# Kernel optimization log

Measured on AMD Instinct MI355X. Metric: run time of the kernel, lower is better.

Reference implementation:

```python
import jax, jax.numpy as jnp
import numpy as np
from jax import lax

VOCAB, ENC_DIM, PRED_H, JOINT_H = 4096, 1024, 640, 640
T, MAX_SYM, BLANK, SOS = 128, 30, 0, -1
S = T * (MAX_SYM + 1)  # upper bound on greedy-decode loop iterations


def setup_inputs() -> dict:
    key = jax.random.key(0)
    ks = jax.random.split(key, 10)
    rn = lambda k, shape, s: jax.random.normal(k, shape, jnp.float32) * s
    return {
        "enc_out": rn(ks[0], (1, T, ENC_DIM), 1.0),
        "out_len": T,
        "emb": rn(ks[1], (VOCAB, PRED_H), 0.1),
        "Wih0": rn(ks[2], (4 * PRED_H, PRED_H), 0.04),
        "Whh0": rn(ks[3], (4 * PRED_H, PRED_H), 0.04),
        "b0": jnp.zeros((4 * PRED_H,), jnp.float32),
        "Wih1": rn(ks[4], (4 * PRED_H, PRED_H), 0.04),
        "Whh1": rn(ks[5], (4 * PRED_H, PRED_H), 0.04),
        "b1": jnp.zeros((4 * PRED_H,), jnp.float32),
        "Wj1": rn(ks[6], (JOINT_H, ENC_DIM + PRED_H), 0.03),
        "bj1": jnp.zeros((JOINT_H,), jnp.float32),
        "Wj2": rn(ks[7], (VOCAB, JOINT_H), 0.04),
        "bj2": jnp.zeros((VOCAB,), jnp.float32),
    }


def _lstm_cell(x, h, c, Wih, Whh, b):
    z = x @ Wih.T + h @ Whh.T + b  # [4H], torch gate order i,f,g,o
    i, f, g, o = jnp.split(z, 4)
    c2 = jax.nn.sigmoid(f) * c + jax.nn.sigmoid(i) * jnp.tanh(g)
    return jax.nn.sigmoid(o) * jnp.tanh(c2), c2


def _decode(enc_out, timesteps, emb, Wih0, Whh0, b0, Wih1, Whh1, b1, Wj1, bj1, Wj2, bj2):
    enc = enc_out[0]  # [T, ENC_DIM]

    def step(carry, _):
        t, sa, last, h0, c0, h1, c1, labels, cnt, done = carry
        # prediction net step (SOS = -1 -> zero embedding)
        g_in = jnp.where(last < 0, 0.0, emb[jnp.maximum(last, 0)])
        h0n, c0n = _lstm_cell(g_in, h0, c0, Wih0, Whh0, b0)
        h1n, c1n = _lstm_cell(h0n, h1, c1, Wih1, Whh1, b1)
        # joint net on current encoder frame
        f = enc[jnp.minimum(t, T - 1)]
        hid = jax.nn.relu(Wj1 @ jnp.concatenate([f, h1n]) + bj1)
        logits = Wj2 @ hid + bj2  # [VOCAB]
        k = jnp.argmax(logits).astype(jnp.int32)
        stop_sym = (k == BLANK) | (sa >= MAX_SYM)
        emit = (~stop_sym) & (~done)
        adv = stop_sym & (~done)
        # emit: append symbol, keep hidden'; blank/max: advance time, discard hidden'
        last2 = jnp.where(emit, k, last)
        h0 = jnp.where(emit, h0n, h0); c0 = jnp.where(emit, c0n, c0)
        h1 = jnp.where(emit, h1n, h1); c1 = jnp.where(emit, c1n, c1)
        labels = labels.at[cnt].set(jnp.where(emit, k, labels[cnt]))
        cnt2 = cnt + emit.astype(jnp.int32)
        sa2 = jnp.where(emit, sa + 1, jnp.where(adv, 0, sa))
        t2 = t + adv.astype(jnp.int32)
        done2 = done | (adv & (t2 >= timesteps))
        out_logits = jnp.where(done, 0.0, logits)
        return (t2, sa2, last2, h0, c0, h1, c1, labels, cnt2, done2), out_logits

    zeros = jnp.zeros((PRED_H,), jnp.float32)
    carry0 = (jnp.int32(0), jnp.int32(0), jnp.int32(SOS),
              zeros, zeros, zeros, zeros,
              jnp.full((S,), -1, jnp.int32), jnp.int32(0), jnp.bool_(False))
    carry, logits_seq = lax.scan(step, carry0, None, length=S)
    labels, cnt = carry[7], carry[8]
    return logits_seq, labels, cnt


def reference(enc_out, out_len, emb, Wih0, Whh0, b0, Wih1, Whh1, b1, Wj1, bj1, Wj2, bj2):
    return _decode(enc_out, out_len, emb, Wih0, Whh0, b0, Wih1, Whh1, b1, Wj1, bj1, Wj2, bj2)
```

## Files before the change

kernel.cpp:

```cpp
#include <hip/hip_runtime.h>
#include <cmath>

#define VOCAB   4096
#define ENC_DIM 1024
#define PRED_H  640
#define JOINT_H 640
#define TMAX    128
#define MAX_SYM 30
#define NSTEPS  (TMAX*(MAX_SYM+1))
#define NWG     160
#define NTHR    512
#define RLX __ATOMIC_RELAXED
#define AGT __HIP_MEMORY_SCOPE_AGENT

typedef unsigned long long u64;
typedef __attribute__((ext_vector_type(4))) float f32x4;
typedef __attribute__((ext_vector_type(4))) unsigned int u32x4;


__device__ __forceinline__ float wave_red(float v){
  v += __shfl_xor(v, 32, 64);
  v += __shfl_xor(v, 16, 64);
  v += __shfl_xor(v,  8, 64);
  v += __shfl_xor(v,  4, 64);
  v += __shfl_xor(v,  2, 64);
  v += __shfl_xor(v,  1, 64);
  return v;
}

__device__ __forceinline__ float sigf(float x){ return 1.0f/(1.0f+expf(-x)); }

__device__ __forceinline__ void sendline(u64* base, int w, f32x4 hv, unsigned tag){
  u32x4 a, b;
  a.x = __float_as_uint(hv.x); a.y = tag; a.z = __float_as_uint(hv.y); a.w = tag;
  b.x = __float_as_uint(hv.z); b.y = tag; b.z = __float_as_uint(hv.w); b.w = tag;
  u64* p = base + ((size_t)w<<3);
  asm volatile("global_store_dwordx4 %0, %2, off sc0 sc1\n\t"
               "global_store_dwordx4 %1, %3, off sc0 sc1"
               :: "v"(p), "v"(p+2), "v"(a), "v"(b) : "memory");
}

__device__ __forceinline__ void pollline(const u64* base, float* dstLDS,
                                         unsigned tag, int i){
  const u64* p = base + ((size_t)i<<3);
  u32x4 v0, v1;
  for(;;){
    asm volatile("global_load_dwordx4 %0, %2, off sc0 sc1\n\t"
                 "global_load_dwordx4 %1, %3, off sc0 sc1\n\t"
                 "s_waitcnt vmcnt(0)"
                 : "=&v"(v0), "=&v"(v1) : "v"(p), "v"(p+2) : "memory");
    if (v0.y == tag && v0.w == tag && v1.y == tag && v1.w == tag) break;
    __builtin_amdgcn_s_sleep(1);
  }
  __builtin_amdgcn_sched_barrier(0);
  float* d = dstLDS + (i<<2);
  d[0] = __uint_as_float(v0.x);
  d[1] = __uint_as_float(v0.z);
  d[2] = __uint_as_float(v1.x);
  d[3] = __uint_as_float(v1.z);
}

__device__ __forceinline__ u64 mkentry(float lg, int r, unsigned ep){
  unsigned u = __float_as_uint(lg);
  u = (u & 0x80000000u) ? ~u : (u | 0x80000000u);
  return ((u64)u<<24) | ((u64)(ep&0xFFFu)<<12) | (u64)(4095 - r);
}

__global__ void init_ws(unsigned* ws){
  for (int i = threadIdx.x; i < 10240; i += 256) ws[i] = 0u;
}

__global__ __launch_bounds__(NTHR, 1)
void rnnt_decode(const float* __restrict__ enc,
                 const int*   __restrict__ outlen_p,
                 const float* __restrict__ emb,
                 const float* __restrict__ Wih0, const float* __restrict__ Whh0, const float* __restrict__ b0,
                 const float* __restrict__ Wih1, const float* __restrict__ Whh1, const float* __restrict__ b1,
                 const float* __restrict__ Wj1,  const float* __restrict__ bj1,
                 const float* __restrict__ Wj2,  const float* __restrict__ bj2,
                 float* __restrict__ out,
                 char* __restrict__ ws)
{
  const int wg = blockIdx.x, tid = threadIdx.x;
  const int wave = tid >> 6, lane = tid & 63;
  const int timesteps = outlen_p[0];

  u64* dataA = (u64*)(ws);
  u64* dataB = (u64*)(ws + 10240);
  u64* dataH = (u64*)(ws + 20480);
  u64* parts = (u64*)(ws + 30720);

  __shared__ float xsh[ENC_DIM];
  __shared__ float h0buf[2][PRED_H];
  __shared__ float h1buf[2][PRED_H];
  __shared__ float hidsh[JOINT_H];
  __shared__ float zsh[4][4];
  __shared__ float zjsA[8], zjsB[8];
  __shared__ float c0c[4], c1c[4], c0p[4], c1p[4];
  __shared__ float bj1sh[4];
  __shared__ u64 psh[8];
  __shared__ u64 pmx[3];

  const int jb = wg*4;

  const int gA = wave & 3;
  const int jA = wave >> 2;
  const int rowA = gA*PRED_H + jb + jA;
  const int rowB = gA*PRED_H + jb + jA + 2;

  float w0xA[10], w0hA[10], w0xB[10], w0hB[10];
  float w1xA[10], w1hA[10], w1xB[10], w1hB[10];
  #pragma unroll
  for (int i = 0; i < 10; ++i){
    int c = lane + (i<<6);
    w0xA[i] = Wih0[(size_t)rowA*PRED_H + c];
    w0hA[i] = Whh0[(size_t)rowA*PRED_H + c];
    w1xA[i] = Wih1[(size_t)rowA*PRED_H + c];
    w1hA[i] = Whh1[(size_t)rowA*PRED_H + c];
    w0xB[i] = Wih0[(size_t)rowB*PRED_H + c];
    w0hB[i] = Whh0[(size_t)rowB*PRED_H + c];
    w1xB[i] = Wih1[(size_t)rowB*PRED_H + c];
    w1hB[i] = Whh1[(size_t)rowB*PRED_H + c];
  }
  const float bA0 = b0[rowA], bA1 = b1[rowA];
  const float bB0 = b0[rowB], bB1 = b1[rowB];

  const int grp = wave >> 2;
  const int vt  = ((wave & 3)<<6) | lane;
  const int rP0 = jb + grp;
  const int rP1 = jb + 2 + grp;
  float wjf0[4], wjh0[3], wjf1[4], wjh1[3];
  #pragma unroll
  for (int i = 0; i < 4; ++i){
    wjf0[i] = Wj1[(size_t)rP0*(ENC_DIM+PRED_H) + vt + (i<<8)];
    wjf1[i] = Wj1[(size_t)rP1*(ENC_DIM+PRED_H) + vt + (i<<8)];
  }
  #pragma unroll
  for (int i = 0; i < 3; ++i){
    int c = vt + (i<<8);
    wjh0[i] = (c < PRED_H) ? Wj1[(size_t)rP0*(ENC_DIM+PRED_H) + ENC_DIM + c] : 0.f;
    wjh1[i] = (c < PRED_H) ? Wj1[(size_t)rP1*(ENC_DIM+PRED_H) + ENC_DIM + c] : 0.f;
  }
  float ca0 = 0.f, ca1 = 0.f;

  const int nrows = (wg < 96) ? 26 : 25;
  const int r2b = wg*25 + (wg < 96 ? wg : 96);
  float wj2[4][10], bj2r[4];
  #pragma unroll
  for (int p = 0; p < 4; ++p){
    bool act = (p*8 + wave) < nrows;
    int r = act ? (r2b + p*8 + wave) : 0;
    #pragma unroll
    for (int i = 0; i < 10; ++i)
      wj2[p][i] = act ? Wj2[(size_t)r*JOINT_H + lane + (i<<6)] : 0.f;
    bj2r[p] = act ? bj2[r] : 0.f;
  }

  for (int i = tid; i < PRED_H; i += NTHR){ h0buf[0][i] = 0.f; h1buf[0][i] = 0.f;
                                            h0buf[1][i] = 0.f; h1buf[1][i] = 0.f; }
  if (tid < 4){ c0c[tid] = 0.f; c1c[tid] = 0.f; bj1sh[tid] = bj1[jb+tid]; }
  __syncthreads();

  int cur = 0, t = 0, sa = 0, last = -1, cnt = 0, tStaged = -1;
  bool done = false, reuse = false;
  float s0A = 0.f, s0B = 0.f, s1A = 0.f, s1B = 0.f;

  for (int s = 0; s < NSTEPS; ++s){
    if (done){
      if (wg < 8) out[(size_t)s*VOCAB + wg*NTHR + tid] = 0.f;
      continue;
    }
    const unsigned tag = (unsigned)(s + 1);

    if (!reuse){
      {
        float XA = 0.f, XB = 0.f;
        if (last >= 0){
          float xr[10];
          #pragma unroll
          for (int i = 0; i < 10; ++i)
            xr[i] = emb[(size_t)last*PRED_H + lane + (i<<6)];
          #pragma unroll
          for (int i = 0; i < 10; ++i){
            XA = fmaf(w0xA[i], xr[i], XA);
            XB = fmaf(w0xB[i], xr[i], XB);
          }
          XA = wave_red(XA);
          XB = wave_red(XB);
        }
        if (lane == 0){
          zsh[gA][jA]   = XA + s0A + bA0;
          zsh[gA][jA+2] = XB + s0B + bB0;
        }
      }
      __syncthreads();
      if (wave == 0){
        float hv = 0.f;
        if (lane < 4){
          float ig = sigf(zsh[0][lane]), fg = sigf(zsh[1][lane]);
          float gg = tanhf(zsh[2][lane]), og = sigf(zsh[3][lane]);
          float c2 = fg*c0c[lane] + ig*gg;
          c0p[lane] = c2;
          hv = og*tanhf(c2);
        }
        f32x4 v;
        v.x = __shfl(hv, 0, 64); v.y = __shfl(hv, 1, 64);
        v.z = __shfl(hv, 2, 64); v.w = __shfl(hv, 3, 64);
        if (lane == 0) sendline(dataA, wg, v, tag);
      }

      if (tid < 160) pollline(dataA, h0buf[cur^1], tag, tid);
      __syncthreads();
      {
        float XA = 0.f, XB = 0.f;
        #pragma unroll
        for (int i = 0; i < 10; ++i){
          float h0 = h0buf[cur^1][lane+(i<<6)];
          XA = fmaf(w1xA[i], h0, XA);
          XB = fmaf(w1xB[i], h0, XB);
        }
        XA = wave_red(XA);
        XB = wave_red(XB);
        if (lane == 0){
          zsh[gA][jA]   = XA + s1A + bA1;
          zsh[gA][jA+2] = XB + s1B + bB1;
        }
      }
      __syncthreads();
      if (wave == 0){
        float hv = 0.f;
        if (lane < 4){
          float ig = sigf(zsh[0][lane]), fg = sigf(zsh[1][lane]);
          float gg = tanhf(zsh[2][lane]), og = sigf(zsh[3][lane]);
          float c2 = fg*c1c[lane] + ig*gg;
          c1p[lane] = c2;
          hv = og*tanhf(c2);
        }
        f32x4 v;
        v.x = __shfl(hv, 0, 64); v.y = __shfl(hv, 1, 64);
        v.z = __shfl(hv, 2, 64); v.w = __shfl(hv, 3, 64);
        if (lane == 0) sendline(dataB, wg, v, tag);
      }
    }

    {
      int tcap = (t < TMAX-1) ? t : (TMAX-1);
      bool fNew = (tcap != tStaged);
      if (fNew)
        for (int i = tid; i < ENC_DIM; i += NTHR) xsh[i] = enc[(size_t)tcap*ENC_DIM + i];
      if (!reuse){
        if (tid < 160) pollline(dataB, h1buf[cur^1], tag, tid);
      }
      __syncthreads();
      if (fNew){
        float a = 0.f, b = 0.f;
        #pragma unroll
        for (int i = 0; i < 4; ++i){
          a = fmaf(wjf0[i], xsh[vt+(i<<8)], a);
          b = fmaf(wjf1[i], xsh[vt+(i<<8)], b);
        }
        ca0 = a; ca1 = b;
        tStaged = tcap;
      }
      {
        float acc = ca0;
        #pragma unroll
        for (int i = 0; i < 3; ++i){
          int c = vt + (i<<8);
          acc = fmaf(wjh0[i], h1buf[cur^1][(c < PRED_H) ? c : 0], acc);
        }
        acc = wave_red(acc);
        if (lane == 0) zjsA[wave] = acc;
        float acc2 = ca1;
        #pragma unroll
        for (int i = 0; i < 3; ++i){
          int c = vt + (i<<8);
          acc2 = fmaf(wjh1[i], h1buf[cur^1][(c < PRED_H) ? c : 0], acc2);
        }
        acc2 = wave_red(acc2);
        if (lane == 0) zjsB[wave] = acc2;
      }
      __syncthreads();
      if (wave == 0){
        float hv = 0.f;
        if (lane < 4){
          float v;
          if (lane == 0)      v = zjsA[0]+zjsA[1]+zjsA[2]+zjsA[3] + bj1sh[0];
          else if (lane == 1) v = zjsA[4]+zjsA[5]+zjsA[6]+zjsA[7] + bj1sh[1];
          else if (lane == 2) v = zjsB[0]+zjsB[1]+zjsB[2]+zjsB[3] + bj1sh[2];
          else                v = zjsB[4]+zjsB[5]+zjsB[6]+zjsB[7] + bj1sh[3];
          hv = v > 0.f ? v : 0.f;
        }
        f32x4 v;
        v.x = __shfl(hv, 0, 64); v.y = __shfl(hv, 1, 64);
        v.z = __shfl(hv, 2, 64); v.w = __shfl(hv, 3, 64);
        if (lane == 0) sendline(dataH, wg, v, tag);
      }
    }

    int k;
    {
      if (tid < 160) pollline(dataH, hidsh, tag, tid);
      __syncthreads();
      u64 best = 0;
      #pragma unroll
      for (int p = 0; p < 4; ++p){
        if (p*8 + wave < nrows){
          int r = r2b + p*8 + wave;
          float acc = 0.f;
          #pragma unroll
          for (int i = 0; i < 10; ++i) acc = fmaf(wj2[p][i], hidsh[lane+(i<<6)], acc);
          acc = wave_red(acc);
          if (lane == 0){
            float lg = acc + bj2r[p];
            out[(size_t)s*VOCAB + r] = lg;
            u64 e = mkentry(lg, r, tag);
            if (e > best) best = e;
          }
        }
      }
      if (lane == 0) psh[wave] = best;
      __syncthreads();
      if (tid == 0){
        u64 m = psh[0];
        #pragma unroll
        for (int w = 1; w < 8; ++w) if (psh[w] > m) m = psh[w];
        __hip_atomic_store(&parts[(size_t)wg<<3], m, RLX, AGT);
      }

      {
        float a0 = 0.f, b0v = 0.f, a1 = 0.f, b1v = 0.f;
        #pragma unroll
        for (int i = 0; i < 10; ++i){
          float h0p = h0buf[cur^1][lane+(i<<6)];
          float h1p = h1buf[cur^1][lane+(i<<6)];
          a0  = fmaf(w0hA[i], h0p, a0);
          b0v = fmaf(w0hB[i], h0p, b0v);
          a1  = fmaf(w1hA[i], h1p, a1);
          b1v = fmaf(w1hB[i], h1p, b1v);
        }
        s0A = wave_red(a0);  s0B = wave_red(b0v);
        s1A = wave_red(a1);  s1B = wave_red(b1v);
      }

      u64 myp = 0;
      if (tid < 160){
        for(;;){
          u64 e = __hip_atomic_load(&parts[(size_t)tid<<3], RLX, AGT);
          if ((unsigned)((e>>12) & 0xFFFu) == (tag & 0xFFFu)){ myp = e; break; }
          __builtin_amdgcn_s_sleep(1);
        }
      }
      if (wave < 3){
        #pragma unroll
        for (int off = 32; off; off >>= 1){
          u64 o = __shfl_xor(myp, off, 64);
          if (o > myp) myp = o;
        }
        if (lane == 0) pmx[wave] = myp;
      }
      __syncthreads();
      u64 m = pmx[0];
      if (pmx[1] > m) m = pmx[1];
      if (pmx[2] > m) m = pmx[2];
      k = 4095 - (int)(m & 0xFFFull);
    }

    bool stop = (k == 0) || (sa >= MAX_SYM);
    if (!stop){
      if (wg == 0 && tid == 0) out[(size_t)NSTEPS*VOCAB + cnt] = (float)k;
      if (tid < 4){ c0c[tid] = c0p[tid]; c1c[tid] = c1p[tid]; }
      cnt++; sa++; last = k; cur ^= 1; reuse = false;
    } else {
      sa = 0; t++; reuse = true;
      if (t >= timesteps) done = true;
    }
    __syncthreads();
  }

  size_t lab = (size_t)NSTEPS*VOCAB;
  int gidx = wg*NTHR + tid;
  for (int i = cnt + gidx; i < NSTEPS; i += NWG*NTHR) out[lab + i] = -1.f;
  if (wg == 0 && tid == 0) out[lab + NSTEPS] = (float)cnt;
}

extern "C" void kernel_launch(void* const* d_in, const int* in_sizes, int n_in,
                              void* d_out, int out_size, void* d_ws, size_t ws_size,
                              hipStream_t stream) {
  const float* enc  = (const float*)d_in[0];
  const int*   olen = (const int*)  d_in[1];
  const float* emb  = (const float*)d_in[2];
  const float* Wih0 = (const float*)d_in[3];
  const float* Whh0 = (const float*)d_in[4];
  const float* b0   = (const float*)d_in[5];
  const float* Wih1 = (const float*)d_in[6];
  const float* Whh1 = (const float*)d_in[7];
  const float* b1   = (const float*)d_in[8];
  const float* Wj1  = (const float*)d_in[9];
  const float* bj1  = (const float*)d_in[10];
  const float* Wj2  = (const float*)d_in[11];
  const float* bj2  = (const float*)d_in[12];
  float* out = (float*)d_out;
  char* ws = (char*)d_ws;

  init_ws<<<1, 256, 0, stream>>>((unsigned*)d_ws);

  void* args[] = {&enc,&olen,&emb,&Wih0,&Whh0,&b0,&Wih1,&Whh1,&b1,
                  &Wj1,&bj1,&Wj2,&bj2,&out,&ws};
  hipLaunchCooperativeKernel((const void*)rnnt_decode, dim3(NWG), dim3(NTHR),
                             args, 0, stream);
}
```

Before: 41.60 ms.

## Cut per-step barriers and serial lanes in cross-workgroup decode exchange

```diff
diff --git a/kernel.cpp b/kernel.cpp
--- a/kernel.cpp
+++ b/kernel.cpp
@@ -14,7 +14,6 @@
 #define AGT __HIP_MEMORY_SCOPE_AGENT
 
 typedef unsigned long long u64;
-typedef __attribute__((ext_vector_type(4))) float f32x4;
 typedef __attribute__((ext_vector_type(4))) unsigned int u32x4;
 
 
@@ -30,14 +29,9 @@
 
 __device__ __forceinline__ float sigf(float x){ return 1.0f/(1.0f+expf(-x)); }
 
-__device__ __forceinline__ void sendline(u64* base, int w, f32x4 hv, unsigned tag){
-  u32x4 a, b;
-  a.x = __float_as_uint(hv.x); a.y = tag; a.z = __float_as_uint(hv.y); a.w = tag;
-  b.x = __float_as_uint(hv.z); b.y = tag; b.z = __float_as_uint(hv.w); b.w = tag;
-  u64* p = base + ((size_t)w<<3);
-  asm volatile("global_store_dwordx4 %0, %2, off sc0 sc1\n\t"
-               "global_store_dwordx4 %1, %3, off sc0 sc1"
-               :: "v"(p), "v"(p+2), "v"(a), "v"(b) : "memory");
+__device__ __forceinline__ void send8(u64* base, int w, int slot, float v, unsigned tag){
+  __hip_atomic_store(base + ((size_t)w<<3) + slot,
+                     ((u64)tag<<32) | (u64)__float_as_uint(v), RLX, AGT);
 }
 
 __device__ __forceinline__ void pollline(const u64* base, float* dstLDS,
@@ -58,6 +52,35 @@
   d[1] = __uint_as_float(v0.z);
   d[2] = __uint_as_float(v1.x);
   d[3] = __uint_as_float(v1.z);
+}
+
+__device__ __forceinline__ u64 pollparts(const u64* base, unsigned tag12, int i){
+  const u64* p = base + ((size_t)i<<3);
+  u32x4 v0, v1, v2, v3;
+  for(;;){
+    asm volatile("global_load_dwordx4 %0, %4, off sc0 sc1\n\t"
+                 "global_load_dwordx4 %1, %5, off sc0 sc1\n\t"
+                 "global_load_dwordx4 %2, %6, off sc0 sc1\n\t"
+                 "global_load_dwordx4 %3, %7, off sc0 sc1\n\t"
+                 "s_waitcnt vmcnt(0)"
+                 : "=&v"(v0),"=&v"(v1),"=&v"(v2),"=&v"(v3)
+                 : "v"(p),"v"(p+2),"v"(p+4),"v"(p+6) : "memory");
+    bool ok = (((v0.x>>12)&0xFFFu)==tag12) & (((v0.z>>12)&0xFFFu)==tag12)
+            & (((v1.x>>12)&0xFFFu)==tag12) & (((v1.z>>12)&0xFFFu)==tag12)
+            & (((v2.x>>12)&0xFFFu)==tag12) & (((v2.z>>12)&0xFFFu)==tag12)
+            & (((v3.x>>12)&0xFFFu)==tag12) & (((v3.z>>12)&0xFFFu)==tag12);
+    if (ok) break;
+    __builtin_amdgcn_s_sleep(1);
+  }
+  u64 m = ((u64)v0.y<<32)|v0.x, e;
+  e = ((u64)v0.w<<32)|v0.z; if (e>m) m=e;
+  e = ((u64)v1.y<<32)|v1.x; if (e>m) m=e;
+  e = ((u64)v1.w<<32)|v1.z; if (e>m) m=e;
+  e = ((u64)v2.y<<32)|v2.x; if (e>m) m=e;
+  e = ((u64)v2.w<<32)|v2.z; if (e>m) m=e;
+  e = ((u64)v3.y<<32)|v3.x; if (e>m) m=e;
+  e = ((u64)v3.w<<32)|v3.z; if (e>m) m=e;
+  return m;
 }
 
 __device__ __forceinline__ u64 mkentry(float lg, int r, unsigned ep){
@@ -91,17 +114,18 @@
   u64* parts = (u64*)(ws + 30720);
 
   __shared__ float xsh[ENC_DIM];
-  __shared__ float h0buf[2][PRED_H];
-  __shared__ float h1buf[2][PRED_H];
+  __shared__ float h0buf[PRED_H];
+  __shared__ float h1buf[PRED_H];
   __shared__ float hidsh[JOINT_H];
   __shared__ float zsh[4][4];
   __shared__ float zjsA[8], zjsB[8];
   __shared__ float c0c[4], c1c[4], c0p[4], c1p[4];
   __shared__ float bj1sh[4];
-  __shared__ u64 psh[8];
   __shared__ u64 pmx[3];
 
   const int jb = wg*4;
+  const int pollid = tid - 256;
+  const bool isPoll = ((unsigned)pollid < 160u);
 
   const int gA = wave & 3;
   const int jA = wave >> 2;
@@ -156,12 +180,11 @@
     bj2r[p] = act ? bj2[r] : 0.f;
   }
 
-  for (int i = tid; i < PRED_H; i += NTHR){ h0buf[0][i] = 0.f; h1buf[0][i] = 0.f;
-                                            h0buf[1][i] = 0.f; h1buf[1][i] = 0.f; }
+  for (int i = tid; i < PRED_H; i += NTHR){ h0buf[i] = 0.f; h1buf[i] = 0.f; }
   if (tid < 4){ c0c[tid] = 0.f; c1c[tid] = 0.f; bj1sh[tid] = bj1[jb+tid]; }
   __syncthreads();
 
-  int cur = 0, t = 0, sa = 0, last = -1, cnt = 0, tStaged = -1;
+  int t = 0, sa = 0, last = -1, cnt = 0, tStaged = -1;
   bool done = false, reuse = false;
   float s0A = 0.f, s0B = 0.f, s1A = 0.f, s1B = 0.f;
 
@@ -194,28 +217,22 @@
         }
       }
       __syncthreads();
-      if (wave == 0){
-        float hv = 0.f;
-        if (lane < 4){
-          float ig = sigf(zsh[0][lane]), fg = sigf(zsh[1][lane]);
-          float gg = tanhf(zsh[2][lane]), og = sigf(zsh[3][lane]);
-          float c2 = fg*c0c[lane] + ig*gg;
-          c0p[lane] = c2;
-          hv = og*tanhf(c2);
-        }
-        f32x4 v;
-        v.x = __shfl(hv, 0, 64); v.y = __shfl(hv, 1, 64);
-        v.z = __shfl(hv, 2, 64); v.w = __shfl(hv, 3, 64);
-        if (lane == 0) sendline(dataA, wg, v, tag);
-      }
-
-      if (tid < 160) pollline(dataA, h0buf[cur^1], tag, tid);
+      if (wave < 4 && lane == 0){
+        int j = wave;
+        float ig = sigf(zsh[0][j]), fg = sigf(zsh[1][j]);
+        float gg = tanhf(zsh[2][j]), og = sigf(zsh[3][j]);
+        float c2 = fg*c0c[j] + ig*gg;
+        c0p[j] = c2;
+        send8(dataA, wg, j, og*tanhf(c2), tag);
+      }
+
+      if (isPoll) pollline(dataA, h0buf, tag, pollid);
       __syncthreads();
       {
         float XA = 0.f, XB = 0.f;
         #pragma unroll
         for (int i = 0; i < 10; ++i){
-          float h0 = h0buf[cur^1][lane+(i<<6)];
+          float h0 = h0buf[lane+(i<<6)];
           XA = fmaf(w1xA[i], h0, XA);
           XB = fmaf(w1xB[i], h0, XB);
         }
@@ -227,30 +244,22 @@
         }
       }
       __syncthreads();
-      if (wave == 0){
-        float hv = 0.f;
-        if (lane < 4){
-          float ig = sigf(zsh[0][lane]), fg = sigf(zsh[1][lane]);
-          float gg = tanhf(zsh[2][lane]), og = sigf(zsh[3][lane]);
-          float c2 = fg*c1c[lane] + ig*gg;
-          c1p[lane] = c2;
-          hv = og*tanhf(c2);
-        }
-        f32x4 v;
-        v.x = __shfl(hv, 0, 64); v.y = __shfl(hv, 1, 64);
-        v.z = __shfl(hv, 2, 64); v.w = __shfl(hv, 3, 64);
-        if (lane == 0) sendline(dataB, wg, v, tag);
+      if (wave < 4 && lane == 0){
+        int j = wave;
+        float ig = sigf(zsh[0][j]), fg = sigf(zsh[1][j]);
+        float gg = tanhf(zsh[2][j]), og = sigf(zsh[3][j]);
+        float c2 = fg*c1c[j] + ig*gg;
+        c1p[j] = c2;
+        send8(dataB, wg, j, og*tanhf(c2), tag);
       }
     }
 
     {
       int tcap = (t < TMAX-1) ? t : (TMAX-1);
       bool fNew = (tcap != tStaged);
-      if (fNew)
-        for (int i = tid; i < ENC_DIM; i += NTHR) xsh[i] = enc[(size_t)tcap*ENC_DIM + i];
-      if (!reuse){
-        if (tid < 160) pollline(dataB, h1buf[cur^1], tag, tid);
-      }
+      if (fNew && tid < 256)
+        for (int i = tid; i < ENC_DIM; i += 256) xsh[i] = enc[(size_t)tcap*ENC_DIM + i];
+      if (!reuse && isPoll) pollline(dataB, h1buf, tag, pollid);
       __syncthreads();
       if (fNew){
         float a = 0.f, b = 0.f;
@@ -267,7 +276,7 @@
         #pragma unroll
         for (int i = 0; i < 3; ++i){
           int c = vt + (i<<8);
-          acc = fmaf(wjh0[i], h1buf[cur^1][(c < PRED_H) ? c : 0], acc);
+          acc = fmaf(wjh0[i], h1buf[(c < PRED_H) ? c : 0], acc);
         }
         acc = wave_red(acc);
         if (lane == 0) zjsA[wave] = acc;
@@ -275,65 +284,62 @@
         #pragma unroll
         for (int i = 0; i < 3; ++i){
           int c = vt + (i<<8);
-          acc2 = fmaf(wjh1[i], h1buf[cur^1][(c < PRED_H) ? c : 0], acc2);
+          acc2 = fmaf(wjh1[i], h1buf[(c < PRED_H) ? c : 0], acc2);
         }
         acc2 = wave_red(acc2);
         if (lane == 0) zjsB[wave] = acc2;
       }
       __syncthreads();
-      if (wave == 0){
-        float hv = 0.f;
-        if (lane < 4){
-          float v;
-          if (lane == 0)      v = zjsA[0]+zjsA[1]+zjsA[2]+zjsA[3] + bj1sh[0];
-          else if (lane == 1) v = zjsA[4]+zjsA[5]+zjsA[6]+zjsA[7] + bj1sh[1];
-          else if (lane == 2) v = zjsB[0]+zjsB[1]+zjsB[2]+zjsB[3] + bj1sh[2];
-          else                v = zjsB[4]+zjsB[5]+zjsB[6]+zjsB[7] + bj1sh[3];
-          hv = v > 0.f ? v : 0.f;
-        }
-        f32x4 v;
-        v.x = __shfl(hv, 0, 64); v.y = __shfl(hv, 1, 64);
-        v.z = __shfl(hv, 2, 64); v.w = __shfl(hv, 3, 64);
-        if (lane == 0) sendline(dataH, wg, v, tag);
+      if (wave < 4 && lane == 0){
+        int j = wave;
+        float v;
+        if (j == 0)      v = zjsA[0]+zjsA[1]+zjsA[2]+zjsA[3] + bj1sh[0];
+        else if (j == 1) v = zjsA[4]+zjsA[5]+zjsA[6]+zjsA[7] + bj1sh[1];
+        else if (j == 2) v = zjsB[0]+zjsB[1]+zjsB[2]+zjsB[3] + bj1sh[2];
+        else             v = zjsB[4]+zjsB[5]+zjsB[6]+zjsB[7] + bj1sh[3];
+        send8(dataH, wg, j, v > 0.f ? v : 0.f, tag);
       }
     }
 
     int k;
     {
-      if (tid < 160) pollline(dataH, hidsh, tag, tid);
-      __syncthreads();
-      u64 best = 0;
-      #pragma unroll
-      for (int p = 0; p < 4; ++p){
-        if (p*8 + wave < nrows){
-          int r = r2b + p*8 + wave;
-          float acc = 0.f;
+      if (isPoll) pollline(dataH, hidsh, tag, pollid);
+      __syncthreads();
+      {
+        float a0 = 0.f, a1 = 0.f, a2 = 0.f, a3 = 0.f;
+        #pragma unroll
+        for (int i = 0; i < 10; ++i){
+          float h = hidsh[lane+(i<<6)];
+          a0 = fmaf(wj2[0][i], h, a0);
+          a1 = fmaf(wj2[1][i], h, a1);
+          a2 = fmaf(wj2[2][i], h, a2);
+          a3 = fmaf(wj2[3][i], h, a3);
+        }
+        a0 = wave_red(a0); a1 = wave_red(a1);
+        a2 = wave_red(a2); a3 = wave_red(a3);
+        if (lane == 0){
+          u64 best = 0;
+          float av[4] = {a0, a1, a2, a3};
           #pragma unroll
-          for (int i = 0; i < 10; ++i) acc = fmaf(wj2[p][i], hidsh[lane+(i<<6)], acc);
-          acc = wave_red(acc);
-          if (lane == 0){
-            float lg = acc + bj2r[p];
-            out[(size_t)s*VOCAB + r] = lg;
-            u64 e = mkentry(lg, r, tag);
-            if (e > best) best = e;
+          for (int p = 0; p < 4; ++p){
+            if (p*8 + wave < nrows){
+              int r = r2b + p*8 + wave;
+              float lg = av[p] + bj2r[p];
+              out[(size_t)s*VOCAB + r] = lg;
+              u64 e = mkentry(lg, r, tag);
+              if (e > best) best = e;
+            }
           }
-        }
-      }
-      if (lane == 0) psh[wave] = best;
-      __syncthreads();
-      if (tid == 0){
-        u64 m = psh[0];
-        #pragma unroll
-        for (int w = 1; w < 8; ++w) if (psh[w] > m) m = psh[w];
-        __hip_atomic_store(&parts[(size_t)wg<<3], m, RLX, AGT);
+          __hip_atomic_store(&parts[((size_t)wg<<3) + wave], best, RLX, AGT);
+        }
       }
 
       {
         float a0 = 0.f, b0v = 0.f, a1 = 0.f, b1v = 0.f;
         #pragma unroll
         for (int i = 0; i < 10; ++i){
-          float h0p = h0buf[cur^1][lane+(i<<6)];
-          float h1p = h1buf[cur^1][lane+(i<<6)];
+          float h0p = h0buf[lane+(i<<6)];
+          float h1p = h1buf[lane+(i<<6)];
           a0  = fmaf(w0hA[i], h0p, a0);
           b0v = fmaf(w0hB[i], h0p, b0v);
           a1  = fmaf(w1hA[i], h1p, a1);
@@ -344,13 +350,7 @@
       }
 
       u64 myp = 0;
-      if (tid < 160){
-        for(;;){
-          u64 e = __hip_atomic_load(&parts[(size_t)tid<<3], RLX, AGT);
-          if ((unsigned)((e>>12) & 0xFFFu) == (tag & 0xFFFu)){ myp = e; break; }
-          __builtin_amdgcn_s_sleep(1);
-        }
-      }
+      if (tid < 160) myp = pollparts(parts, tag & 0xFFFu, tid);
       if (wave < 3){
         #pragma unroll
         for (int off = 32; off; off >>= 1){
@@ -370,12 +370,11 @@
     if (!stop){
       if (wg == 0 && tid == 0) out[(size_t)NSTEPS*VOCAB + cnt] = (float)k;
       if (tid < 4){ c0c[tid] = c0p[tid]; c1c[tid] = c1p[tid]; }
-      cnt++; sa++; last = k; cur ^= 1; reuse = false;
+      cnt++; sa++; last = k; reuse = false;
     } else {
       sa = 0; t++; reuse = true;
       if (t >= timesteps) done = true;
     }
-    __syncthreads();
   }
 
   size_t lab = (size_t)NSTEPS*VOCAB;
```

After: 50.52 ms. +21.4%, slower.

## Single-buffer hidden state, move polling to upper waves, fuse Wj2 row loop

Applied to the files above, without the earlier changes.

```diff
diff --git a/kernel.cpp b/kernel.cpp
--- a/kernel.cpp
+++ b/kernel.cpp
@@ -91,8 +91,8 @@
   u64* parts = (u64*)(ws + 30720);
 
   __shared__ float xsh[ENC_DIM];
-  __shared__ float h0buf[2][PRED_H];
-  __shared__ float h1buf[2][PRED_H];
+  __shared__ float h0buf[PRED_H];
+  __shared__ float h1buf[PRED_H];
   __shared__ float hidsh[JOINT_H];
   __shared__ float zsh[4][4];
   __shared__ float zjsA[8], zjsB[8];
@@ -102,6 +102,8 @@
   __shared__ u64 pmx[3];
 
   const int jb = wg*4;
+  const int pollid = tid - 256;
+  const bool isPoll = ((unsigned)pollid < 160u);
 
   const int gA = wave & 3;
   const int jA = wave >> 2;
@@ -156,12 +158,11 @@
     bj2r[p] = act ? bj2[r] : 0.f;
   }
 
-  for (int i = tid; i < PRED_H; i += NTHR){ h0buf[0][i] = 0.f; h1buf[0][i] = 0.f;
-                                            h0buf[1][i] = 0.f; h1buf[1][i] = 0.f; }
+  for (int i = tid; i < PRED_H; i += NTHR){ h0buf[i] = 0.f; h1buf[i] = 0.f; }
   if (tid < 4){ c0c[tid] = 0.f; c1c[tid] = 0.f; bj1sh[tid] = bj1[jb+tid]; }
   __syncthreads();
 
-  int cur = 0, t = 0, sa = 0, last = -1, cnt = 0, tStaged = -1;
+  int t = 0, sa = 0, last = -1, cnt = 0, tStaged = -1;
   bool done = false, reuse = false;
   float s0A = 0.f, s0B = 0.f, s1A = 0.f, s1B = 0.f;
 
@@ -209,13 +210,13 @@
         if (lane == 0) sendline(dataA, wg, v, tag);
       }
 
-      if (tid < 160) pollline(dataA, h0buf[cur^1], tag, tid);
+      if (isPoll) pollline(dataA, h0buf, tag, pollid);
       __syncthreads();
       {
         float XA = 0.f, XB = 0.f;
         #pragma unroll
         for (int i = 0; i < 10; ++i){
-          float h0 = h0buf[cur^1][lane+(i<<6)];
+          float h0 = h0buf[lane+(i<<6)];
           XA = fmaf(w1xA[i], h0, XA);
           XB = fmaf(w1xB[i], h0, XB);
         }
@@ -249,7 +250,7 @@
       if (fNew)
         for (int i = tid; i < ENC_DIM; i += NTHR) xsh[i] = enc[(size_t)tcap*ENC_DIM + i];
       if (!reuse){
-        if (tid < 160) pollline(dataB, h1buf[cur^1], tag, tid);
+        if (isPoll) pollline(dataB, h1buf, tag, pollid);
       }
       __syncthreads();
       if (fNew){
@@ -267,7 +268,7 @@
         #pragma unroll
         for (int i = 0; i < 3; ++i){
           int c = vt + (i<<8);
-          acc = fmaf(wjh0[i], h1buf[cur^1][(c < PRED_H) ? c : 0], acc);
+          acc = fmaf(wjh0[i], h1buf[(c < PRED_H) ? c : 0], acc);
         }
         acc = wave_red(acc);
         if (lane == 0) zjsA[wave] = acc;
@@ -275,7 +276,7 @@
         #pragma unroll
         for (int i = 0; i < 3; ++i){
           int c = vt + (i<<8);
-          acc2 = fmaf(wjh1[i], h1buf[cur^1][(c < PRED_H) ? c : 0], acc2);
+          acc2 = fmaf(wjh1[i], h1buf[(c < PRED_H) ? c : 0], acc2);
         }
         acc2 = wave_red(acc2);
         if (lane == 0) zjsB[wave] = acc2;
@@ -300,26 +301,36 @@
 
     int k;
     {
-      if (tid < 160) pollline(dataH, hidsh, tag, tid);
-      __syncthreads();
-      u64 best = 0;
-      #pragma unroll
-      for (int p = 0; p < 4; ++p){
-        if (p*8 + wave < nrows){
-          int r = r2b + p*8 + wave;
-          float acc = 0.f;
+      if (isPoll) pollline(dataH, hidsh, tag, pollid);
+      __syncthreads();
+      {
+        float a0 = 0.f, a1 = 0.f, a2 = 0.f, a3 = 0.f;
+        #pragma unroll
+        for (int i = 0; i < 10; ++i){
+          float h = hidsh[lane+(i<<6)];
+          a0 = fmaf(wj2[0][i], h, a0);
+          a1 = fmaf(wj2[1][i], h, a1);
+          a2 = fmaf(wj2[2][i], h, a2);
+          a3 = fmaf(wj2[3][i], h, a3);
+        }
+        a0 = wave_red(a0); a1 = wave_red(a1);
+        a2 = wave_red(a2); a3 = wave_red(a3);
+        if (lane == 0){
+          u64 best = 0;
+          float av[4] = {a0, a1, a2, a3};
           #pragma unroll
-          for (int i = 0; i < 10; ++i) acc = fmaf(wj2[p][i], hidsh[lane+(i<<6)], acc);
-          acc = wave_red(acc);
-          if (lane == 0){
-            float lg = acc + bj2r[p];
-            out[(size_t)s*VOCAB + r] = lg;
-            u64 e = mkentry(lg, r, tag);
-            if (e > best) best = e;
+          for (int p = 0; p < 4; ++p){
+            if (p*8 + wave < nrows){
+              int r = r2b + p*8 + wave;
+              float lg = av[p] + bj2r[p];
+              out[(size_t)s*VOCAB + r] = lg;
+              u64 e = mkentry(lg, r, tag);
+              if (e > best) best = e;
+            }
           }
-        }
-      }
-      if (lane == 0) psh[wave] = best;
+          psh[wave] = best;
+        }
+      }
       __syncthreads();
       if (tid == 0){
         u64 m = psh[0];
@@ -332,8 +343,8 @@
         float a0 = 0.f, b0v = 0.f, a1 = 0.f, b1v = 0.f;
         #pragma unroll
         for (int i = 0; i < 10; ++i){
-          float h0p = h0buf[cur^1][lane+(i<<6)];
-          float h1p = h1buf[cur^1][lane+(i<<6)];
+          float h0p = h0buf[lane+(i<<6)];
+          float h1p = h1buf[lane+(i<<6)];
           a0  = fmaf(w0hA[i], h0p, a0);
           b0v = fmaf(w0hB[i], h0p, b0v);
           a1  = fmaf(w1hA[i], h1p, a1);
@@ -370,12 +381,11 @@
     if (!stop){
       if (wg == 0 && tid == 0) out[(size_t)NSTEPS*VOCAB + cnt] = (float)k;
       if (tid < 4){ c0c[tid] = c0p[tid]; c1c[tid] = c1p[tid]; }
-      cnt++; sa++; last = k; cur ^= 1; reuse = false;
+      cnt++; sa++; last = k; reuse = false;
     } else {
       sa = 0; t++; reuse = true;
       if (t >= timesteps) done = true;
     }
-    __syncthreads();
   }
 
   size_t lab = (size_t)NSTEPS*VOCAB;
```

Result: no change. 41.03 ms, median of 2 (-1.4%).
